# Optimization experiments

Measured on AMD Instinct MI355X. Metric: run time of the kernel, lower is better.

Reference implementation:

```python
import jax, jax.numpy as jnp
import numpy as np

CHUNK_SIZE = 256


def setup_inputs() -> dict:
    key = jax.random.key(0)
    kq, kk, kv = jax.random.split(key, 3)
    b, h, L, d, dv = 2, 16, 4096, 16, 64
    return {
        "q": jax.random.normal(kq, (b, h, L, d), dtype=jnp.float32),
        "k": jax.random.normal(kk, (b, h, L, d), dtype=jnp.float32),
        "v": jax.random.normal(kv, (b, h, L, dv), dtype=jnp.float32),
    }


def reference(q, k, v):
    b, h, L, d = q.shape
    dv = v.shape[-1]
    cs = CHUNK_SIZE
    n = L // cs

    q = q * d ** (-0.5)

    # ---- normalizer z over full sequence ----
    k_cumsum = jnp.cumsum(k, axis=-2)                               # [b,h,L,d]
    kk_cumsum = jnp.cumsum(k[..., :, None] * k[..., None, :], axis=-3)  # [b,h,L,d,d]
    z = (q * k_cumsum).sum(-1)
    z = z + 0.5 * jnp.einsum('bhld,bhle,bhlde->bhl', q, q, kk_cumsum)
    z = z + (jnp.arange(L, dtype=z.dtype) + 1.0)[None, None, :]

    # ---- zeroth-order term ----
    o_const = jnp.cumsum(v, axis=-2)                                # [b,h,L,dv]

    # ---- chunked view ----
    qc = q.reshape(b, h, n, cs, d)
    kc = k.reshape(b, h, n, cs, d)
    vc = v.reshape(b, h, n, cs, dv)

    # intra-chunk quadratic attention: S + 0.5*S^2, causal-masked
    s = jnp.einsum('bhnqd,bhnkd->bhnqk', qc, kc)                    # [b,h,n,cs,cs]
    s = s + 0.5 * s ** 2
    causal_mask = jnp.tril(jnp.ones((cs, cs), dtype=bool))
    s = jnp.where(causal_mask, s, jnp.zeros((), dtype=s.dtype))
    o = jnp.einsum('bhnqk,bhnkf->bhnqf', s, vc)                     # [b,h,n,cs,dv]

    # inter-chunk quadratic state: cumulative K x K x V from previous chunks
    kv_quad = jnp.einsum('bhncd,bhnce,bhncf->bhndef', kc, kc, vc)   # [b,h,n,d,d,dv]
    kv_quad = jnp.cumsum(kv_quad, axis=2)
    kv_quad = jnp.concatenate(
        [jnp.zeros_like(kv_quad[:, :, :1]), kv_quad[:, :, :-1]], axis=2)
    o = o + 0.5 * jnp.einsum('bhndef,bhncd,bhnce->bhncf', kv_quad, qc, qc)

    # inter-chunk linear state: cumulative K x V from previous chunks
    kv_lin = jnp.einsum('bhncd,bhnce->bhnde', kc, vc)               # [b,h,n,d,dv]
    kv_lin = jnp.cumsum(kv_lin, axis=2)
    kv_lin = jnp.concatenate(
        [jnp.zeros_like(kv_lin[:, :, :1]), kv_lin[:, :, :-1]], axis=2)
    o = o + jnp.einsum('bhnde,bhncd->bhnce', kv_lin, qc)

    o = o.reshape(b, h, L, dv) + o_const
    return o / (z[..., None] + 1e-6)
```

## Files before the change

kernel.cpp:

```cpp
#include <hip/hip_runtime.h>
#include <cstddef>

#define BH    32
#define LSEQ  4096
#define D     16
#define DV    64
#define CS    256
#define NC    16
#define NF    160
#define NZ    65
#define KSTEPS 5
#define PER   (NZ * NF)

typedef short short8 __attribute__((ext_vector_type(8)));
typedef float f32x4 __attribute__((ext_vector_type(4)));
typedef float f4 __attribute__((ext_vector_type(4)));
typedef unsigned uint4v __attribute__((ext_vector_type(4)));

#define OFF_KBF 0u
#define OFF_ST  (4u*1024u*1024u)

__device__ __forceinline__ float bf2f(unsigned short u) {
  return __uint_as_float(((unsigned)u) << 16);
}
__device__ __forceinline__ short8 zero8() {
  short8 z = {0,0,0,0,0,0,0,0};
  return z;
}
__device__ __forceinline__ unsigned cvtpk(float lo, float hi) {
  unsigned r;
  asm("v_cvt_pk_bf16_f32 %0, %1, %2" : "=v"(r) : "v"(lo), "v"(hi));
  return r;
}
__device__ __forceinline__ short8 pk4(unsigned a, unsigned b, unsigned c, unsigned d) {
  uint4v u = {a, b, c, d};
  return __builtin_bit_cast(short8, u);
}

__device__ __forceinline__ int vtc(int f, int j) {
  return (j + (((f >> 2) & 7) << 3)) & 255;
}

__device__ __forceinline__ unsigned feat_tbl(int f) {
  if (f == 0)  return 16u | (16u << 8);
  if (f <= 16) return (unsigned)(f - 1) | (16u << 8);
  if (f < 137) {
    int p = f - 17, off = 0;
    for (int d = 0; d < 15; ++d) {
      int cnt = 15 - d;
      if (p < off + cnt) return (unsigned)d | ((unsigned)(d + 1 + p - off) << 8);
      off += cnt;
    }
  }
  if (f < 153) {
    int d = f - 137;
    return (unsigned)d | ((unsigned)d << 8) | (1u << 16);
  }
  return 17u | (17u << 8);
}

__global__ __launch_bounds__(512, 4) void pass1(const float* __restrict__ k,
                                                const float* __restrict__ v,
                                                unsigned* __restrict__ kbf_u32,
                                                unsigned short* __restrict__ st) {
  __shared__ float kx[CS][18];
  __shared__ __align__(16) unsigned short vt[NZ][264];
  __shared__ unsigned tbl[NF];
  int blk = blockIdx.x, bh = blk & 31, c = blk >> 5;
  int t = threadIdx.x, w = t >> 6, lane = t & 63, quad = lane >> 4, n16 = lane & 15;
  const size_t base = (size_t)bh * LSEQ + (size_t)c * CS;
  (void)lane;

  {
    const f4* K4 = (const f4*)(k + base * D);
    uint2* kbd2 = (uint2*)(kbf_u32 + base * D / 2);
    for (int idx = t; idx < 1024; idx += 512) {
      f4 kv = K4[idx];
      kbd2[idx] = make_uint2(cvtpk(kv[0], kv[1]), cvtpk(kv[2], kv[3]));
      float* dst = &kx[idx >> 2][(idx & 3) * 4];
      *(float2*)dst = make_float2(kv[0], kv[1]);
      *(float2*)(dst + 2) = make_float2(kv[2], kv[3]);
    }
    for (int i = t; i < CS; i += 512) { kx[i][16] = 1.f; kx[i][17] = 0.f; }
  }
  if (c < 15) {
    const f4* V4 = (const f4*)(v + base * DV);
    for (int idx = t; idx < 2048; idx += 512) {
      int m16 = idx & 15, j0 = (idx >> 4) * 2;
      f4 a  = V4[j0 * 16 + m16];
      f4 bq = V4[j0 * 16 + 16 + m16];
#pragma unroll
      for (int r = 0; r < 4; ++r)
        *(unsigned*)&vt[m16 * 4 + r][vtc(m16 * 4 + r, j0)] = cvtpk(a[r], bq[r]);
    }
    if (t < 128) ((unsigned*)&vt[64][0])[t] = 0x3F803F80u;
  }
  if (t < NF) tbl[t] = feat_tbl(t);
  __syncthreads();

  if (c < 15) {
    const int ntt = (w < 2) ? 2 : 1;
    unsigned short* stc = st + (size_t)(bh * NC + c) * PER;
    for (int tt = 0; tt < ntt; ++tt) {
      const int T = tt ? (w + 8) : w;
      unsigned tv = tbl[T * 16 + n16];
      int d0 = tv & 255, e0 = (tv >> 8) & 255;
      f32x4 acc5[5];
#pragma unroll
      for (int nt = 0; nt < 5; ++nt) acc5[nt] = (f32x4){0.f, 0.f, 0.f, 0.f};
      for (int jt = 0; jt < 8; ++jt) {
        float x[8];
#pragma unroll
        for (int i = 0; i < 8; ++i) {
          const float* kr = &kx[jt * 32 + quad * 8 + i][0];
          x[i] = kr[d0] * kr[e0];
        }
        short8 afr = pk4(cvtpk(x[0], x[1]), cvtpk(x[2], x[3]),
                         cvtpk(x[4], x[5]), cvtpk(x[6], x[7]));
#pragma unroll
        for (int nt = 0; nt < 5; ++nt) {
          int ncol = nt * 16 + n16;
          short8 b = zero8();
          if (ncol < NZ)
            b = *(const short8*)(&vt[ncol][vtc(ncol, jt * 32 + quad * 8)]);
          acc5[nt] = __builtin_amdgcn_mfma_f32_16x16x32_bf16(afr, b, acc5[nt], 0, 0, 0);
        }
      }
      const int feat0 = T * 16 + quad * 4;
      float sc[4];
#pragma unroll
      for (int r = 0; r < 4; ++r)
        sc[r] = (feat0 + r >= 137 && feat0 + r < 153) ? 0.5f : 1.0f;
#pragma unroll
      for (int nt = 0; nt < 5; ++nt) {
        int col = nt * 16 + n16;
        if (col < NZ) {
          unsigned lo = cvtpk(acc5[nt][0] * sc[0], acc5[nt][1] * sc[1]);
          unsigned hi = cvtpk(acc5[nt][2] * sc[2], acc5[nt][3] * sc[3]);
          *(uint2*)(stc + (size_t)col * NF + feat0) = make_uint2(lo, hi);
        }
      }
    }
  }
}

struct Smem2 {
  float qx[CS][18];
  __align__(16) unsigned short vt[NZ][264];
  union {
    __align__(16) unsigned short stt[NZ][168];
    struct {
      __align__(16) unsigned short ptile[8][640];
      float zline[CS];
    } u;
  } b;
  unsigned tbl[NF];
};

__global__ __launch_bounds__(512, 4) void pass2(const float* __restrict__ q,
                                                const unsigned short* __restrict__ kbf,
                                                const float* __restrict__ v,
                                                const unsigned short* __restrict__ st,
                                                float* __restrict__ out) {
  __shared__ Smem2 sm;
  int blk = blockIdx.x, bh = blk & 31, c = blk >> 5;
  int t = threadIdx.x, w = t >> 6, lane = t & 63, quad = lane >> 4, n16 = lane & 15;
  const size_t base = (size_t)bh * LSEQ + (size_t)c * CS;

  const int s0 = w;
  const int s1 = 15 - w;

  short8 qf[2] = {zero8(), zero8()};
  if (quad < 2) {
#pragma unroll
    for (int mm = 0; mm < 2; ++mm) {
      int s = mm ? s1 : s0;
      const f4* qp = (const f4*)(q + (base + (size_t)(s * 16 + n16)) * D + quad * 8);
      f4 qa = qp[0] * 0.25f;
      f4 qb = qp[1] * 0.25f;
      qf[mm] = pk4(cvtpk(qa[0], qa[1]), cvtpk(qa[2], qa[3]),
                   cvtpk(qb[0], qb[1]), cvtpk(qb[2], qb[3]));
    }
  }

  {
    const f4* Q4 = (const f4*)(q + base * D);
    for (int idx = t; idx < 1024; idx += 512) {
      f4 qv = Q4[idx] * 0.25f;
      float* dst = &sm.qx[idx >> 2][(idx & 3) * 4];
      *(float2*)dst = make_float2(qv[0], qv[1]);
      *(float2*)(dst + 2) = make_float2(qv[2], qv[3]);
    }
    for (int i = t; i < CS; i += 512) { sm.qx[i][16] = 1.f; sm.qx[i][17] = 0.f; }
    const f4* V4 = (const f4*)(v + base * DV);
    for (int idx = t; idx < 2048; idx += 512) {
      int m16 = idx & 15, j0 = (idx >> 4) * 2;
      f4 a  = V4[j0 * 16 + m16];
      f4 bq = V4[j0 * 16 + 16 + m16];
#pragma unroll
      for (int r = 0; r < 4; ++r)
        *(unsigned*)&sm.vt[m16 * 4 + r][vtc(m16 * 4 + r, j0)] = cvtpk(a[r], bq[r]);
    }
    if (t < 128) ((unsigned*)&sm.vt[64][0])[t] = 0x3F803F80u;
    if (t < NF) sm.tbl[t] = feat_tbl(t);
  }
  __syncthreads();

  if (c > 0) {
    const unsigned short* stg = st + (size_t)bh * NC * PER;
    float sa0[8], sa1[8], sa2[8];
#pragma unroll
    for (int e = 0; e < 8; ++e) { sa0[e] = 0.f; sa1[e] = 0.f; sa2[e] = 0.f; }
    const int i0 = t * 8, i1 = i0 + 4096, i2 = i0 + 8192;
    const bool h2 = (i2 < PER);
    short8 a0 = *(const short8*)(stg + i0);
    short8 a1 = *(const short8*)(stg + i1);
    short8 a2 = h2 ? *(const short8*)(stg + i2) : zero8();
    for (int cc = 1; cc < c; ++cc) {
      const unsigned short* pn = stg + (size_t)cc * PER;
      short8 b0 = *(const short8*)(pn + i0);
      short8 b1 = *(const short8*)(pn + i1);
      short8 b2 = h2 ? *(const short8*)(pn + i2) : zero8();
#pragma unroll
      for (int e = 0; e < 8; ++e) {
        sa0[e] += bf2f((unsigned short)a0[e]);
        sa1[e] += bf2f((unsigned short)a1[e]);
        sa2[e] += bf2f((unsigned short)a2[e]);
      }
      a0 = b0; a1 = b1; a2 = b2;
    }
#pragma unroll
    for (int e = 0; e < 8; ++e) {
      sa0[e] += bf2f((unsigned short)a0[e]);
      sa1[e] += bf2f((unsigned short)a1[e]);
      sa2[e] += bf2f((unsigned short)a2[e]);
    }
    {
      int col = i0 / NF, ft = i0 - col * NF;
      *(short8*)(&sm.b.stt[col][ft]) =
          pk4(cvtpk(sa0[0], sa0[1]), cvtpk(sa0[2], sa0[3]),
              cvtpk(sa0[4], sa0[5]), cvtpk(sa0[6], sa0[7]));
      col = i1 / NF; ft = i1 - col * NF;
      *(short8*)(&sm.b.stt[col][ft]) =
          pk4(cvtpk(sa1[0], sa1[1]), cvtpk(sa1[2], sa1[3]),
              cvtpk(sa1[4], sa1[5]), cvtpk(sa1[6], sa1[7]));
      if (h2) {
        col = i2 / NF; ft = i2 - col * NF;
        *(short8*)(&sm.b.stt[col][ft]) =
            pk4(cvtpk(sa2[0], sa2[1]), cvtpk(sa2[2], sa2[3]),
                cvtpk(sa2[4], sa2[5]), cvtpk(sa2[6], sa2[7]));
      }
    }
  }
  __syncthreads();

  f32x4 accC[2][5];
#pragma unroll
  for (int mm = 0; mm < 2; ++mm)
#pragma unroll
    for (int nt = 0; nt < 5; ++nt) accC[mm][nt] = (f32x4){0.f, 0.f, 0.f, 0.f};

  if (c > 0) {
    const float* qrow0 = &sm.qx[s0 * 16 + n16][0];
    const float* qrow1 = &sm.qx[s1 * 16 + n16][0];
    for (int ks = 0; ks < KSTEPS; ++ks) {
      unsigned tvv[8];
#pragma unroll
      for (int i = 0; i < 8; ++i) tvv[i] = sm.tbl[ks * 32 + quad * 8 + i];
      float x0[8], x1[8];
#pragma unroll
      for (int i = 0; i < 8; ++i) {
        int d = tvv[i] & 255, e = (tvv[i] >> 8) & 255;
        x0[i] = qrow0[d] * qrow0[e];
        x1[i] = qrow1[d] * qrow1[e];
      }
      short8 afr0 = pk4(cvtpk(x0[0], x0[1]), cvtpk(x0[2], x0[3]),
                        cvtpk(x0[4], x0[5]), cvtpk(x0[6], x0[7]));
      short8 afr1 = pk4(cvtpk(x1[0], x1[1]), cvtpk(x1[2], x1[3]),
                        cvtpk(x1[4], x1[5]), cvtpk(x1[6], x1[7]));
#pragma unroll
      for (int nt = 0; nt < 5; ++nt) {
        int ncol = nt * 16 + n16;
        short8 b = zero8();
        if (ncol < NZ) b = *(const short8*)(&sm.b.stt[ncol][ks * 32 + quad * 8]);
        accC[0][nt] = __builtin_amdgcn_mfma_f32_16x16x32_bf16(afr0, b, accC[0][nt], 0, 0, 0);
        accC[1][nt] = __builtin_amdgcn_mfma_f32_16x16x32_bf16(afr1, b, accC[1][nt], 0, 0, 0);
      }
    }
  }
  __syncthreads();

  const unsigned short* kbc = kbf + base * D;
  unsigned short* pw = &sm.b.u.ptile[w][0];
  short8 ones;
#pragma unroll
  for (int i = 0; i < 8; ++i) ones[i] = (short)0x3F80;

#pragma unroll
  for (int mm = 0; mm < 2; ++mm) {
    const int s = mm ? s1 : s0;
    const int ntiles = (s >> 1) + 1;
    for (int jt = 0; jt < ntiles; ++jt) {
      short8 kb[2];
#pragma unroll
      for (int ntk = 0; ntk < 2; ++ntk) {
        short8 b = zero8();
        if (quad < 2)
          b = *(const short8*)(kbc + (size_t)(jt * 32 + ntk * 16 + n16) * D + quad * 8);
        kb[ntk] = b;
      }
      f32x4 zf = (f32x4){0.f, 0.f, 0.f, 0.f};
      f32x4 sres[2];
      sres[0] = __builtin_amdgcn_mfma_f32_16x16x32_bf16(qf[mm], kb[0], zf, 0, 0, 0);
      sres[1] = __builtin_amdgcn_mfma_f32_16x16x32_bf16(qf[mm], kb[1], zf, 0, 0, 0);
      const bool last = (jt == ntiles - 1);
#pragma unroll
      for (int ntk = 0; ntk < 2; ++ntk) {
        float ph[4];
#pragma unroll
        for (int r = 0; r < 4; ++r) {
          float sv = sres[ntk][r];
          float phi = fmaf(sv, fmaf(0.5f, sv, 1.0f), 1.0f);
          if (last) {
            int qrow_g = s * 16 + quad * 4 + r;
            int kcol_g = jt * 32 + ntk * 16 + n16;
            if (kcol_g > qrow_g) phi = 0.f;
          }
          ph[r] = phi;
        }
        unsigned u01 = cvtpk(ph[0], ph[1]);
        unsigned u23 = cvtpk(ph[2], ph[3]);
        int rb = (quad * 4) * 40 + ntk * 16 + n16;
        pw[rb      ] = (unsigned short)u01;
        pw[rb +  40] = (unsigned short)(u01 >> 16);
        pw[rb +  80] = (unsigned short)u23;
        pw[rb + 120] = (unsigned short)(u23 >> 16);
      }
      short8 pa = *(const short8*)(pw + n16 * 40 + quad * 8);
#pragma unroll
      for (int nt = 0; nt < 5; ++nt) {
        int ncol = nt * 16 + n16;
        short8 b;
        if (ncol < 64)
          b = *(const short8*)(&sm.vt[ncol][vtc(ncol, jt * 32 + quad * 8)]);
        else if (ncol == 64) b = ones;
        else                 b = zero8();
        accC[mm][nt] = __builtin_amdgcn_mfma_f32_16x16x32_bf16(pa, b, accC[mm][nt], 0, 0, 0);
      }
    }
  }

  if (n16 == 0) {
#pragma unroll
    for (int mm = 0; mm < 2; ++mm) {
      int s = mm ? s1 : s0;
#pragma unroll
      for (int r = 0; r < 4; ++r)
        sm.b.u.zline[s * 16 + quad * 4 + r] = accC[mm][4][r];
    }
  }
  float* oc = out + base * DV;
#pragma unroll
  for (int mm = 0; mm < 2; ++mm) {
    int s = mm ? s1 : s0;
#pragma unroll
    for (int r = 0; r < 4; ++r) {
      int qrow = s * 16 + quad * 4 + r;
      float inv = __builtin_amdgcn_rcpf(sm.b.u.zline[qrow] + 1e-6f);
#pragma unroll
      for (int nt = 0; nt < 4; ++nt)
        oc[(size_t)qrow * DV + nt * 16 + n16] = accC[mm][nt][r] * inv;
    }
  }
}

extern "C" void kernel_launch(void* const* d_in, const int* in_sizes, int n_in,
                              void* d_out, int out_size, void* d_ws, size_t ws_size,
                              hipStream_t stream) {
  (void)in_sizes; (void)n_in; (void)out_size; (void)ws_size;
  const float* q = (const float*)d_in[0];
  const float* k = (const float*)d_in[1];
  const float* v = (const float*)d_in[2];
  float* out = (float*)d_out;
  char* wsb = (char*)d_ws;
  unsigned*       kbf32 = (unsigned*)(wsb + OFF_KBF);
  unsigned short* kbf   = (unsigned short*)(wsb + OFF_KBF);
  unsigned short* stp   = (unsigned short*)(wsb + OFF_ST);

  pass1<<<BH * NC, 512, 0, stream>>>(k, v, kbf32, stp);
  pass2<<<BH * NC, 512, 0, stream>>>(q, kbf, v, stp, out);
}
```

Before: 123.3 us.

## Precompute transposed bf16 V in pass1 and prefetch inputs before state reduction in pass2

Pass1 now transposes V to bf16 for every chunk, including the last one, and writes the swizzled LDS tile to a global workspace. Pass2 loads that bf16 tile directly instead of re-reading fp32 V and converting it. Pass2 also issues the Q and V loads into registers before the serial prefix-sum loop over chunk states, so their latency overlaps with that loop, and writes them to LDS afterwards. The cost is extra workspace writes in pass1, higher register pressure in pass2, and an added dependency on the workspace layout.

New measurement: 125.2 us. Within noise of the previous version (+1.6%).

```diff
diff --git a/kernel.cpp b/kernel.cpp
--- a/kernel.cpp
+++ b/kernel.cpp
@@ -19,6 +19,7 @@
 
 #define OFF_KBF 0u
 #define OFF_ST  (4u*1024u*1024u)
+#define OFF_VTG (OFF_ST + (unsigned)(BH*NC*PER*2))
 
 __device__ __forceinline__ float bf2f(unsigned short u) {
   return __uint_as_float(((unsigned)u) << 16);
@@ -62,6 +63,7 @@
 __global__ __launch_bounds__(512, 4) void pass1(const float* __restrict__ k,
                                                 const float* __restrict__ v,
                                                 unsigned* __restrict__ kbf_u32,
+                                                unsigned* __restrict__ vtg,
                                                 unsigned short* __restrict__ st) {
   __shared__ float kx[CS][18];
   __shared__ __align__(16) unsigned short vt[NZ][264];
@@ -83,7 +85,7 @@
     }
     for (int i = t; i < CS; i += 512) { kx[i][16] = 1.f; kx[i][17] = 0.f; }
   }
-  if (c < 15) {
+  {
     const f4* V4 = (const f4*)(v + base * DV);
     for (int idx = t; idx < 2048; idx += 512) {
       int m16 = idx & 15, j0 = (idx >> 4) * 2;
@@ -97,6 +99,14 @@
   }
   if (t < NF) tbl[t] = feat_tbl(t);
   __syncthreads();
+
+  {
+    unsigned* dst = vtg + (size_t)bh * NZ * (LSEQ / 2) + (size_t)c * (CS / 2);
+    for (int i = t; i < NZ * (CS / 2); i += 512) {
+      int f = i >> 7, j = i & 127;
+      dst[(size_t)f * (LSEQ / 2) + j] = ((const unsigned*)&vt[f][0])[j];
+    }
+  }
 
   if (c < 15) {
     const int ntt = (w < 2) ? 2 : 1;
@@ -159,7 +169,7 @@
 
 __global__ __launch_bounds__(512, 4) void pass2(const float* __restrict__ q,
                                                 const unsigned short* __restrict__ kbf,
-                                                const float* __restrict__ v,
+                                                const unsigned* __restrict__ vtg,
                                                 const unsigned short* __restrict__ st,
                                                 float* __restrict__ out) {
   __shared__ Smem2 sm;
@@ -183,36 +193,26 @@
     }
   }
 
-  {
-    const f4* Q4 = (const f4*)(q + base * D);
-    for (int idx = t; idx < 1024; idx += 512) {
-      f4 qv = Q4[idx] * 0.25f;
-      float* dst = &sm.qx[idx >> 2][(idx & 3) * 4];
-      *(float2*)dst = make_float2(qv[0], qv[1]);
-      *(float2*)(dst + 2) = make_float2(qv[2], qv[3]);
-    }
-    for (int i = t; i < CS; i += 512) { sm.qx[i][16] = 1.f; sm.qx[i][17] = 0.f; }
-    const f4* V4 = (const f4*)(v + base * DV);
-    for (int idx = t; idx < 2048; idx += 512) {
-      int m16 = idx & 15, j0 = (idx >> 4) * 2;
-      f4 a  = V4[j0 * 16 + m16];
-      f4 bq = V4[j0 * 16 + 16 + m16];
-#pragma unroll
-      for (int r = 0; r < 4; ++r)
-        *(unsigned*)&sm.vt[m16 * 4 + r][vtc(m16 * 4 + r, j0)] = cvtpk(a[r], bq[r]);
-    }
-    if (t < 128) ((unsigned*)&sm.vt[64][0])[t] = 0x3F803F80u;
-    if (t < NF) sm.tbl[t] = feat_tbl(t);
-  }
-  __syncthreads();
-
+  const f4* Q4 = (const f4*)(q + base * D);
+  f4 qs0 = Q4[t];
+  f4 qs1 = Q4[t + 512];
+  const unsigned* vsrc = vtg + (size_t)bh * NZ * (LSEQ / 2) + (size_t)c * (CS / 2);
+  unsigned vs[16];
+#pragma unroll
+  for (int i = 0; i < 16; ++i) {
+    int idx = t + i * 512;
+    vs[i] = vsrc[(size_t)(idx >> 7) * (LSEQ / 2) + (idx & 127)];
+  }
+  unsigned vtail = 0;
+  if (t < 128) vtail = vsrc[(size_t)64 * (LSEQ / 2) + t];
+
+  float sa0[8], sa1[8], sa2[8];
+#pragma unroll
+  for (int e = 0; e < 8; ++e) { sa0[e] = 0.f; sa1[e] = 0.f; sa2[e] = 0.f; }
+  const int i0 = t * 8, i1 = i0 + 4096, i2 = i0 + 8192;
+  const bool h2 = (i2 < PER);
   if (c > 0) {
     const unsigned short* stg = st + (size_t)bh * NC * PER;
-    float sa0[8], sa1[8], sa2[8];
-#pragma unroll
-    for (int e = 0; e < 8; ++e) { sa0[e] = 0.f; sa1[e] = 0.f; sa2[e] = 0.f; }
-    const int i0 = t * 8, i1 = i0 + 4096, i2 = i0 + 8192;
-    const bool h2 = (i2 < PER);
     short8 a0 = *(const short8*)(stg + i0);
     short8 a1 = *(const short8*)(stg + i1);
     short8 a2 = h2 ? *(const short8*)(stg + i2) : zero8();
@@ -235,21 +235,41 @@
       sa1[e] += bf2f((unsigned short)a1[e]);
       sa2[e] += bf2f((unsigned short)a2[e]);
     }
-    {
-      int col = i0 / NF, ft = i0 - col * NF;
+  }
+
+  {
+    f4 qv0 = qs0 * 0.25f;
+    float* d0p = &sm.qx[t >> 2][(t & 3) * 4];
+    *(float2*)d0p = make_float2(qv0[0], qv0[1]);
+    *(float2*)(d0p + 2) = make_float2(qv0[2], qv0[3]);
+    int t1 = t + 512;
+    f4 qv1 = qs1 * 0.25f;
+    float* d1p = &sm.qx[t1 >> 2][(t1 & 3) * 4];
+    *(float2*)d1p = make_float2(qv1[0], qv1[1]);
+    *(float2*)(d1p + 2) = make_float2(qv1[2], qv1[3]);
+    if (t < CS) { sm.qx[t][16] = 1.f; sm.qx[t][17] = 0.f; }
+#pragma unroll
+    for (int i = 0; i < 16; ++i) {
+      int idx = t + i * 512;
+      ((unsigned*)&sm.vt[idx >> 7][0])[idx & 127] = vs[i];
+    }
+    if (t < 128) ((unsigned*)&sm.vt[64][0])[t] = vtail;
+    if (t < NF) sm.tbl[t] = feat_tbl(t);
+  }
+  if (c > 0) {
+    int col = i0 / NF, ft = i0 - col * NF;
+    *(short8*)(&sm.b.stt[col][ft]) =
+        pk4(cvtpk(sa0[0], sa0[1]), cvtpk(sa0[2], sa0[3]),
+            cvtpk(sa0[4], sa0[5]), cvtpk(sa0[6], sa0[7]));
+    col = i1 / NF; ft = i1 - col * NF;
+    *(short8*)(&sm.b.stt[col][ft]) =
+        pk4(cvtpk(sa1[0], sa1[1]), cvtpk(sa1[2], sa1[3]),
+            cvtpk(sa1[4], sa1[5]), cvtpk(sa1[6], sa1[7]));
+    if (h2) {
+      col = i2 / NF; ft = i2 - col * NF;
       *(short8*)(&sm.b.stt[col][ft]) =
-          pk4(cvtpk(sa0[0], sa0[1]), cvtpk(sa0[2], sa0[3]),
-              cvtpk(sa0[4], sa0[5]), cvtpk(sa0[6], sa0[7]));
-      col = i1 / NF; ft = i1 - col * NF;
-      *(short8*)(&sm.b.stt[col][ft]) =
-          pk4(cvtpk(sa1[0], sa1[1]), cvtpk(sa1[2], sa1[3]),
-              cvtpk(sa1[4], sa1[5]), cvtpk(sa1[6], sa1[7]));
-      if (h2) {
-        col = i2 / NF; ft = i2 - col * NF;
-        *(short8*)(&sm.b.stt[col][ft]) =
-            pk4(cvtpk(sa2[0], sa2[1]), cvtpk(sa2[2], sa2[3]),
-                cvtpk(sa2[4], sa2[5]), cvtpk(sa2[6], sa2[7]));
-      }
+          pk4(cvtpk(sa2[0], sa2[1]), cvtpk(sa2[2], sa2[3]),
+              cvtpk(sa2[4], sa2[5]), cvtpk(sa2[6], sa2[7]));
     }
   }
   __syncthreads();
@@ -292,9 +312,6 @@
 
   const unsigned short* kbc = kbf + base * D;
   unsigned short* pw = &sm.b.u.ptile[w][0];
-  short8 ones;
-#pragma unroll
-  for (int i = 0; i < 8; ++i) ones[i] = (short)0x3F80;
 
 #pragma unroll
   for (int mm = 0; mm < 2; ++mm) {
@@ -340,11 +357,9 @@
 #pragma unroll
       for (int nt = 0; nt < 5; ++nt) {
         int ncol = nt * 16 + n16;
-        short8 b;
-        if (ncol < 64)
+        short8 b = zero8();
+        if (ncol < NZ)
           b = *(const short8*)(&sm.vt[ncol][vtc(ncol, jt * 32 + quad * 8)]);
-        else if (ncol == 64) b = ones;
-        else                 b = zero8();
         accC[mm][nt] = __builtin_amdgcn_mfma_f32_16x16x32_bf16(pa, b, accC[mm][nt], 0, 0, 0);
       }
     }
@@ -386,7 +401,8 @@
   unsigned*       kbf32 = (unsigned*)(wsb + OFF_KBF);
   unsigned short* kbf   = (unsigned short*)(wsb + OFF_KBF);
   unsigned short* stp   = (unsigned short*)(wsb + OFF_ST);
-
-  pass1<<<BH * NC, 512, 0, stream>>>(k, v, kbf32, stp);
-  pass2<<<BH * NC, 512, 0, stream>>>(q, kbf, v, stp, out);
-}
+  unsigned*       vtg   = (unsigned*)(wsb + OFF_VTG);
+
+  pass1<<<BH * NC, 512, 0, stream>>>(k, v, kbf32, vtg, stp);
+  pass2<<<BH * NC, 512, 0, stream>>>(q, kbf, vtg, stp, out);
+}
```
